# Kernel tuning notes

Measured on AMD Instinct MI355X. Metric: run time of the kernel, lower is better.

Reference implementation:

```python
import jax, jax.numpy as jnp
import numpy as np

H, D, L, G = 4, 32, 2, 512   # heads, head_dim, conv layers, num graphs
HC = H * D                    # hidden_channels = 128


def _mlp3(x, ws, bs):
    # PyG-style MLP, 3 layers, relu between (no act after last), dropout=0
    for i in range(3):
        x = x @ ws[i] + bs[i]
        if i < 2:
            x = jax.nn.relu(x)
    return x


def _attend(q_dst, k_src, v_src, edge, a_rel_et, m_rel_et, p_rel_et, n_dst):
    """One HGTConv edge-type: relation transform, per-dst segment softmax, scatter.
    q_dst: [Nd,H,D], k_src/v_src: [Ns,H,D], edge: [2,E] (src,dst)."""
    src, dst = edge[0], edge[1]
    k_t = jnp.einsum('nhd,hde->nhe', k_src, a_rel_et)   # relation-specific key
    v_t = jnp.einsum('nhd,hde->nhe', v_src, m_rel_et)   # relation-specific value
    alpha = (q_dst[dst] * k_t[src]).sum(-1) * p_rel_et / jnp.sqrt(jnp.float32(D))  # [E,H]
    amax = jax.ops.segment_max(alpha, dst, num_segments=n_dst)
    amax = jnp.where(jnp.isfinite(amax), amax, 0.0)      # nodes with no in-edges
    ex = jnp.exp(alpha - amax[dst])
    den = jax.ops.segment_sum(ex, dst, num_segments=n_dst)
    w = ex / den[dst]                                    # segment softmax weights
    out = jax.ops.segment_sum(v_t[src] * w[..., None], dst, num_segments=n_dst)
    return out.reshape(n_dst, HC)


def _forward(x_var, x_con, mlp_in_w, mlp_in_b,
             mlp_out_w0, mlp_out_b0, mlp_out_w1, mlp_out_b1, mlp_out_w2, mlp_out_b2,
             k_w, k_b, q_w, q_b, v_w, v_b, a_w, a_b, skip,
             a_rel, m_rel, p_rel, edge_vc, edge_cv, batch_var):
    Nv, Nc = x_var.shape[0], x_con.shape[0]
    # per-node-type input MLPs (nt 0 = variable, nt 1 = constraint)
    xs = [_mlp3(x_var, mlp_in_w[0], mlp_in_b[0]),
          _mlp3(x_con, mlp_in_w[1], mlp_in_b[1])]
    ns = [Nv, Nc]
    for l in range(L):  # HGTConv layers
        k = [(xs[t] @ k_w[l, t] + k_b[l, t]).reshape(ns[t], H, D) for t in (0, 1)]
        q = [(xs[t] @ q_w[l, t] + q_b[l, t]).reshape(ns[t], H, D) for t in (0, 1)]
        v = [(xs[t] @ v_w[l, t] + v_b[l, t]).reshape(ns[t], H, D) for t in (0, 1)]
        # edge type 0: variable -> constraint ; edge type 1: constraint -> variable
        agg_con = _attend(q[1], k[0], v[0], edge_vc, a_rel[l, 0], m_rel[l, 0], p_rel[l, 0], Nc)
        agg_var = _attend(q[0], k[1], v[1], edge_cv, a_rel[l, 1], m_rel[l, 1], p_rel[l, 1], Nv)
        # group='mean' over incoming edge types (one per dst type here), then a_lin + gated skip
        new_xs = []
        for t, agg in ((0, agg_var), (1, agg_con)):
            out = jax.nn.gelu(agg, approximate=False) @ a_w[l, t] + a_b[l, t]
            g = jax.nn.sigmoid(skip[l, t])
            new_xs.append(g * out + (1.0 - g) * xs[t])
        xs = new_xs
    # output head on 'variable' nodes: MLP -> softmax(dim=1) -> global mean pool
    logits = _mlp3(xs[0], [mlp_out_w0, mlp_out_w1, mlp_out_w2], [mlp_out_b0, mlp_out_b1, mlp_out_b2])
    probs = jax.nn.softmax(logits, axis=1)
    summ = jax.ops.segment_sum(probs, batch_var, num_segments=G)
    cnt = jax.ops.segment_sum(jnp.ones((xs[0].shape[0],), probs.dtype), batch_var, num_segments=G)
    return summ / jnp.maximum(cnt, 1.0)[:, None]


def setup_inputs() -> dict:
    key = jax.random.key(0)
    ks = jax.random.split(key, 24)
    Nv = Nc = 50000
    E = 400000
    s = 1.0 / np.sqrt(HC)  # fan-in scale for hidden-width linears
    sd = 1.0 / np.sqrt(D)
    inp = {
        'x_var': jax.random.normal(ks[0], (Nv, HC), jnp.float32),
        'x_con': jax.random.normal(ks[1], (Nc, HC), jnp.float32),
        'mlp_in_w': jax.random.normal(ks[2], (2, 3, HC, HC), jnp.float32) * s,
        'mlp_in_b': jnp.zeros((2, 3, HC), jnp.float32),
        'mlp_out_w0': jax.random.normal(ks[3], (HC, HC), jnp.float32) * s,
        'mlp_out_b0': jnp.zeros((HC,), jnp.float32),
        'mlp_out_w1': jax.random.normal(ks[4], (HC, HC), jnp.float32) * s,
        'mlp_out_b1': jnp.zeros((HC,), jnp.float32),
        'mlp_out_w2': jax.random.normal(ks[5], (HC, 2), jnp.float32) * s,
        'mlp_out_b2': jnp.zeros((2,), jnp.float32),
        'k_w': jax.random.normal(ks[6], (L, 2, HC, HC), jnp.float32) * s,
        'k_b': jnp.zeros((L, 2, HC), jnp.float32),
        'q_w': jax.random.normal(ks[7], (L, 2, HC, HC), jnp.float32) * s,
        'q_b': jnp.zeros((L, 2, HC), jnp.float32),
        'v_w': jax.random.normal(ks[8], (L, 2, HC, HC), jnp.float32) * s,
        'v_b': jnp.zeros((L, 2, HC), jnp.float32),
        'a_w': jax.random.normal(ks[9], (L, 2, HC, HC), jnp.float32) * s,
        'a_b': jnp.zeros((L, 2, HC), jnp.float32),
        'skip': jnp.ones((L, 2), jnp.float32),
        'a_rel': jax.random.normal(ks[10], (L, 2, H, D, D), jnp.float32) * sd,
        'm_rel': jax.random.normal(ks[11], (L, 2, H, D, D), jnp.float32) * sd,
        'p_rel': jnp.ones((L, 2, H), jnp.float32),
        'edge_vc': jnp.stack([jax.random.randint(ks[12], (E,), 0, Nv, jnp.int32),
                              jax.random.randint(ks[13], (E,), 0, Nc, jnp.int32)]),
        'edge_cv': jnp.stack([jax.random.randint(ks[14], (E,), 0, Nc, jnp.int32),
                              jax.random.randint(ks[15], (E,), 0, Nv, jnp.int32)]),
        'batch_var': jnp.sort(jax.random.randint(ks[16], (Nv,), 0, G, jnp.int32)),
    }
    return inp


def reference(x_var, x_con, mlp_in_w, mlp_in_b,
              mlp_out_w0, mlp_out_b0, mlp_out_w1, mlp_out_b1, mlp_out_w2, mlp_out_b2,
              k_w, k_b, q_w, q_b, v_w, v_b, a_w, a_b, skip,
              a_rel, m_rel, p_rel, edge_vc, edge_cv, batch_var):
    return _forward(x_var, x_con, mlp_in_w, mlp_in_b,
                    mlp_out_w0, mlp_out_b0, mlp_out_w1, mlp_out_b1, mlp_out_w2, mlp_out_b2,
                    k_w, k_b, q_w, q_b, v_w, v_b, a_w, a_b, skip,
                    a_rel, m_rel, p_rel, edge_vc, edge_cv, batch_var)
```

## Files before the change

kernel.cpp:

```cpp
#include <hip/hip_runtime.h>
#include <cstddef>
#include <cstdint>

typedef __attribute__((ext_vector_type(8))) short short8;
typedef __attribute__((ext_vector_type(4))) float float4v;
typedef __attribute__((ext_vector_type(2))) float float2v;
typedef __attribute__((ext_vector_type(2))) __bf16 bf162;

__device__ __forceinline__ float bf2f_lo(unsigned int u) {
    union { unsigned int i; float f; } v; v.i = u << 16; return v.f;
}
__device__ __forceinline__ float bf2f_hi(unsigned int u) {
    union { unsigned int i; float f; } v; v.i = u & 0xFFFF0000u; return v.f;
}
__device__ __forceinline__ unsigned short f2bf(float f) {
    union { float f; unsigned int i; } v; v.f = f;
    unsigned int x = v.i;
    unsigned int r = (x + 0x7FFFu + ((x >> 16) & 1u)) >> 16;
    return (unsigned short)r;
}
__device__ __forceinline__ float geluf(float x) {
    return 0.5f * x * (1.0f + erff(x * 0.70710678118654752f));
}
__device__ __forceinline__ float dot2bf(unsigned int a, unsigned int b, float c) {
#if defined(__has_builtin) && __has_builtin(__builtin_amdgcn_fdot2_f32_bf16)
    union U { unsigned int u; bf162 v; };
    U ua, ub; ua.u = a; ub.u = b;
    return __builtin_amdgcn_fdot2_f32_bf16(ua.v, ub.v, c, false);
#else
    return c + bf2f_lo(a) * bf2f_lo(b) + bf2f_hi(a) * bf2f_hi(b);
#endif
}
__device__ __forceinline__ unsigned int gate_pack(unsigned int nu, unsigned int ou,
                                                  float2v g2, float2v og2) {
    float2v n = {bf2f_lo(nu), bf2f_hi(nu)};
    float2v o = {bf2f_lo(ou), bf2f_hi(ou)};
    float2v r = n * g2 + o * og2;
    return (unsigned int)f2bf(r.x) | ((unsigned int)f2bf(r.y) << 16);
}

__global__ void k_zero(int* __restrict__ p, int n) {
    int i = blockIdx.x * 256 + threadIdx.x;
    if (i < n) p[i] = 0;
}

__global__ void k_swz(const float* __restrict__ mlp_in_w, const float* __restrict__ q_w,
                      const float* __restrict__ a_w, const float* __restrict__ mow0,
                      const float* __restrict__ mow1, const float* __restrict__ mow2,
                      const float* __restrict__ kw, const float* __restrict__ kb,
                      const float* __restrict__ vw, const float* __restrict__ vb,
                      const float* __restrict__ arel, const float* __restrict__ mrel,
                      const float* __restrict__ prel,
                      unsigned short* __restrict__ Wswz, float* __restrict__ Bkv) {
    int idx = blockIdx.y;
    int f = blockIdx.x * 256 + threadIdx.x;
    if (idx == 25) {
        if (f >= 1024) return;
        int lt = f >> 8, c = f & 255;
        int sec = c >> 7, cc = c & 127, h = cc >> 5, e = cc & 31;
        const float* B = sec ? vb : kb;
        const float* R = sec ? mrel : arel;
        float scale = sec ? 1.f : prel[lt * 4 + h] * 0.17677669529663687f;
        const float* rp = R + (size_t)(lt * 4 + h) * 1024 + e;
        const float* bp = B + lt * 128 + h * 32;
        float s = 0.f;
        #pragma unroll 8
        for (int d = 0; d < 32; ++d) s += bp[d] * rp[(size_t)d * 32];
        Bkv[lt * 256 + c] = s * scale;
        return;
    }
    if (f >= 16384) return;
    int j = f & 7, l = (f >> 3) & 63, t = (f >> 9) & 7, sb = f >> 12;
    int k = sb * 32 + (l >> 4) * 8 + j;
    int n = t * 16 + (l & 15);
    float val;
    if (idx < 6)        val = mlp_in_w[(size_t)idx * 16384 + (size_t)k * 128 + n];
    else if (idx < 10)  val = q_w[(size_t)(idx - 6) * 16384 + (size_t)k * 128 + n];
    else if (idx < 14)  val = a_w[(size_t)(idx - 10) * 16384 + (size_t)k * 128 + n];
    else if (idx == 14) val = mow0[(size_t)k * 128 + n];
    else if (idx == 15) val = mow1[(size_t)k * 128 + n];
    else if (idx < 24) {
        int u = idx - 16, lt = u >> 1, sec = u & 1;
        int h = n >> 5, e = n & 31;
        const float* W = sec ? vw : kw;
        const float* R = sec ? mrel : arel;
        float scale = sec ? 1.f : prel[lt * 4 + h] * 0.17677669529663687f;
        const float* rp = R + (size_t)(lt * 4 + h) * 1024 + e;
        const float* wp = W + (size_t)lt * 16384 + (size_t)k * 128 + h * 32;
        float s = 0.f;
        #pragma unroll 8
        for (int d = 0; d < 32; ++d) s += wp[d] * rp[(size_t)d * 32];
        val = s * scale;
    } else val = (n < 2) ? mow2[(size_t)k * 2 + n] : 0.f;
    Wswz[(size_t)idx * 16384 + f] = f2bf(val);
}

__device__ __forceinline__ void stageB(const unsigned short* __restrict__ Wu,
                                       unsigned short* __restrict__ Bst, int tid) {
    #pragma unroll
    for (int k = 0; k < 8; ++k)
        ((uint4*)Bst)[tid + k * 256] = ((const uint4*)Wu)[tid + k * 256];
}

__device__ __forceinline__ void unit_ldst(const short8 av[4], const unsigned short* __restrict__ Bst,
                                          int lane, float4v acc[8]) {
    #pragma unroll
    for (int t = 0; t < 8; ++t) acc[t] = (float4v){0.f, 0.f, 0.f, 0.f};
    #pragma unroll
    for (int s = 0; s < 4; ++s)
        #pragma unroll
        for (int t = 0; t < 8; ++t) {
            short8 bv = *(const short8*)&Bst[(s * 8 + t) * 512 + lane * 8];
            acc[t] = __builtin_amdgcn_mfma_f32_16x16x32_bf16(av[s], bv, acc[t], 0, 0, 0);
        }
}

__global__ __launch_bounds__(256) void k_mlp3qkv(
    const float* __restrict__ Xa, const float* __restrict__ Xb,
    const unsigned short* __restrict__ Wswz, const float* __restrict__ mlp_in_b,
    const float* __restrict__ q_b, const float* __restrict__ Bkv,
    unsigned short* __restrict__ curS, unsigned short* __restrict__ Qs,
    unsigned short* __restrict__ KVs, int NT, int Nv, int Bv) {
    __shared__ unsigned short Bst[16384];
    __shared__ unsigned short tr[4][16][136];
    const int tid = threadIdx.x;
    const int lane = tid & 63, wave = tid >> 6;
    const int quad = lane >> 4, mrow = lane & 15;
    int bx = blockIdx.x;
    int base, end, type;
    if (bx < Bv) { base = bx * 64; end = Nv; type = 0; }
    else         { base = Nv + (bx - Bv) * 64; end = NT; type = 1; }
    const int mbase = base + wave * 16;
    int r0 = mbase + mrow; if (r0 >= end) r0 = end - 1;
    const bool rok = (mbase + mrow) < end;
    const float* ap = (type == 0 ? Xa + (size_t)r0 * 128
                                 : Xb + (size_t)(r0 - Nv) * 128) + quad * 8;
    short8 av[4];
    #pragma unroll
    for (int s = 0; s < 4; ++s) {
        float4 f0 = *(const float4*)(ap + s * 32);
        float4 f1 = *(const float4*)(ap + s * 32 + 4);
        short8 a;
        a[0] = (short)f2bf(f0.x); a[1] = (short)f2bf(f0.y);
        a[2] = (short)f2bf(f0.z); a[3] = (short)f2bf(f0.w);
        a[4] = (short)f2bf(f1.x); a[5] = (short)f2bf(f1.y);
        a[6] = (short)f2bf(f1.z); a[7] = (short)f2bf(f1.w);
        av[s] = a;
    }
    const float* bs = mlp_in_b + type * 384;
    #pragma unroll
    for (int layer = 0; layer < 3; ++layer) {
        __syncthreads();
        stageB(Wswz + (size_t)(type * 3 + layer) * 16384, Bst, tid);
        __syncthreads();
        float4v acc[8];
        unit_ldst(av, Bst, lane, acc);
        const float* b = bs + layer * 128;
        bool relu = layer < 2;
        #pragma unroll
        for (int t = 0; t < 8; ++t) {
            int col = t * 16 + mrow;
            float bb = b[col];
            #pragma unroll
            for (int r = 0; r < 4; ++r) {
                float v = acc[t][r] + bb;
                if (relu) v = fmaxf(v, 0.f);
                tr[wave][quad * 4 + r][col] = f2bf(v);
            }
        }
        #pragma unroll
        for (int s = 0; s < 4; ++s)
            av[s] = *(const short8*)&tr[wave][mrow][s * 32 + quad * 8];
    }
    if (rok) {
        #pragma unroll
        for (int s = 0; s < 4; ++s)
            *(uint4*)(curS + (size_t)r0 * 128 + quad * 8 + s * 32) = *(uint4*)&av[s];
    }
    #pragma unroll
    for (int u = 0; u < 3; ++u) {
        int unit = (u == 0) ? (6 + type) : (16 + type * 2 + (u - 1));
        __syncthreads();
        stageB(Wswz + (size_t)unit * 16384, Bst, tid);
        __syncthreads();
        float4v acc[8];
        unit_ldst(av, Bst, lane, acc);
        const float* bias = (u == 0) ? (q_b + type * 128) : (Bkv + type * 256 + (u - 1) * 128);
        unsigned short* C = (u == 0) ? Qs : KVs;
        const int ldC = (u == 0) ? 128 : 256;
        const int cb = (u == 0) ? 0 : (u - 1) * 128;
        #pragma unroll
        for (int t = 0; t < 8; ++t) {
            int col = t * 16 + mrow;
            float b = bias[col];
            #pragma unroll
            for (int r = 0; r < 4; ++r) {
                int row = mbase + quad * 4 + r;
                if (row < end) C[(size_t)row * ldC + cb + col] = f2bf(acc[t][r] + b);
            }
        }
    }
}

__global__ __launch_bounds__(256) void k_alinqkv(
    const unsigned short* __restrict__ Aagg, const unsigned short* __restrict__ Wswz,
    const float* __restrict__ a_b, const float* __restrict__ skipP,
    const float* __restrict__ q_b, const float* __restrict__ Bkv,
    unsigned short* __restrict__ curS, unsigned short* __restrict__ Qs,
    unsigned short* __restrict__ KVs, int NT, int Nv, int Bv) {
    __shared__ unsigned short Bst[16384];
    __shared__ unsigned short tr[4][16][136];
    const int tid = threadIdx.x;
    const int lane = tid & 63, wave = tid >> 6;
    const int quad = lane >> 4, mrow = lane & 15;
    int bx = blockIdx.x;
    int base, end, type;
    if (bx < Bv) { base = bx * 64; end = Nv; type = 0; }
    else         { base = Nv + (bx - Bv) * 64; end = NT; type = 1; }
    const int mbase = base + wave * 16;
    int r0 = mbase + mrow; if (r0 >= end) r0 = end - 1;
    const bool rok = (mbase + mrow) < end;
    const int ltA = type;
    const int ltQ = 2 + type;
    short8 av[4];
    {
        const unsigned short* ap = Aagg + (size_t)r0 * 128 + quad * 8;
        #pragma unroll
        for (int s = 0; s < 4; ++s) av[s] = *(const short8*)(ap + s * 32);
    }
    {
        __syncthreads();
        stageB(Wswz + (size_t)(10 + ltA) * 16384, Bst, tid);
        __syncthreads();
        float4v acc[8];
        unit_ldst(av, Bst, lane, acc);
        const float* b = a_b + ltA * 128;
        #pragma unroll
        for (int t = 0; t < 8; ++t) {
            int col = t * 16 + mrow;
            float bb = b[col];
            #pragma unroll
            for (int r = 0; r < 4; ++r)
                tr[wave][quad * 4 + r][col] = f2bf(acc[t][r] + bb);
        }
    }
    {
        float gg = 1.f / (1.f + __expf(-skipP[ltA]));
        float2v g2 = {gg, gg}, og2 = {1.f - gg, 1.f - gg};
        #pragma unroll
        for (int s = 0; s < 4; ++s) {
            short8 nv = *(const short8*)&tr[wave][mrow][s * 32 + quad * 8];
            uint4 nu = *(uint4*)&nv;
            uint4 ou = *(const uint4*)(curS + (size_t)r0 * 128 + quad * 8 + s * 32);
            uint4 res;
            res.x = gate_pack(nu.x, ou.x, g2, og2);
            res.y = gate_pack(nu.y, ou.y, g2, og2);
            res.z = gate_pack(nu.z, ou.z, g2, og2);
            res.w = gate_pack(nu.w, ou.w, g2, og2);
            if (rok) *(uint4*)(curS + (size_t)r0 * 128 + quad * 8 + s * 32) = res;
            av[s] = *(short8*)&res;
        }
    }
    #pragma unroll
    for (int u = 0; u < 3; ++u) {
        int unit = (u == 0) ? (6 + ltQ) : (16 + ltQ * 2 + (u - 1));
        __syncthreads();
        stageB(Wswz + (size_t)unit * 16384, Bst, tid);
        __syncthreads();
        float4v acc[8];
        unit_ldst(av, Bst, lane, acc);
        const float* bias = (u == 0) ? (q_b + ltQ * 128) : (Bkv + ltQ * 256 + (u - 1) * 128);
        unsigned short* C = (u == 0) ? Qs : KVs;
        const int ldC = (u == 0) ? 128 : 256;
        const int cb = (u == 0) ? 0 : (u - 1) * 128;
        #pragma unroll
        for (int t = 0; t < 8; ++t) {
            int col = t * 16 + mrow;
            float b = bias[col];
            #pragma unroll
            for (int r = 0; r < 4; ++r) {
                int row = mbase + quad * 4 + r;
                if (row < end) C[(size_t)row * ldC + cb + col] = f2bf(acc[t][r] + b);
            }
        }
    }
}

__global__ __launch_bounds__(256) void k_alinhead(
    const unsigned short* __restrict__ Aagg, const unsigned short* __restrict__ Wswz,
    const float* __restrict__ a_b, const float* __restrict__ skipP,
    const unsigned short* __restrict__ curS,
    const float* __restrict__ mob0, const float* __restrict__ mob1,
    const float* __restrict__ mob2, const int* __restrict__ batch,
    int N, int G, float* __restrict__ gsum, float* __restrict__ gcnt) {
    __shared__ unsigned short Bst[16384];
    __shared__ unsigned short tr[4][16][136];
    __shared__ float sb[64][3];
    const int tid = threadIdx.x;
    const int lane = tid & 63, wave = tid >> 6;
    const int quad = lane >> 4, mrow = lane & 15;
    for (int i = tid; i < 192; i += 256) ((float*)sb)[i] = 0.f;
    const int base = blockIdx.x * 64;
    const int mbase = base + wave * 16;
    int r0 = mbase + mrow; if (r0 >= N) r0 = N - 1;
    const int bmin = batch[base < N ? base : N - 1];
    short8 av[4];
    {
        const unsigned short* ap = Aagg + (size_t)r0 * 128 + quad * 8;
        #pragma unroll
        for (int s = 0; s < 4; ++s) av[s] = *(const short8*)(ap + s * 32);
    }
    {
        __syncthreads();
        stageB(Wswz + (size_t)12 * 16384, Bst, tid);
        __syncthreads();
        float4v acc[8];
        unit_ldst(av, Bst, lane, acc);
        const float* b = a_b + 2 * 128;
        #pragma unroll
        for (int t = 0; t < 8; ++t) {
            int col = t * 16 + mrow;
            float bb = b[col];
            #pragma unroll
            for (int r = 0; r < 4; ++r)
                tr[wave][quad * 4 + r][col] = f2bf(acc[t][r] + bb);
        }
    }
    {
        float gg = 1.f / (1.f + __expf(-skipP[2]));
        float2v g2 = {gg, gg}, og2 = {1.f - gg, 1.f - gg};
        #pragma unroll
        for (int s = 0; s < 4; ++s) {
            short8 nv = *(const short8*)&tr[wave][mrow][s * 32 + quad * 8];
            uint4 nu = *(uint4*)&nv;
            uint4 ou = *(const uint4*)(curS + (size_t)r0 * 128 + quad * 8 + s * 32);
            uint4 res;
            res.x = gate_pack(nu.x, ou.x, g2, og2);
            res.y = gate_pack(nu.y, ou.y, g2, og2);
            res.z = gate_pack(nu.z, ou.z, g2, og2);
            res.w = gate_pack(nu.w, ou.w, g2, og2);
            av[s] = *(short8*)&res;
        }
    }
    #pragma unroll
    for (int layer = 0; layer < 2; ++layer) {
        __syncthreads();
        stageB(Wswz + (size_t)(14 + layer) * 16384, Bst, tid);
        __syncthreads();
        float4v acc[8];
        unit_ldst(av, Bst, lane, acc);
        const float* b = layer ? mob1 : mob0;
        #pragma unroll
        for (int t = 0; t < 8; ++t) {
            int col = t * 16 + mrow;
            float bb = b[col];
            #pragma unroll
            for (int r = 0; r < 4; ++r)
                tr[wave][quad * 4 + r][col] = f2bf(fmaxf(acc[t][r] + bb, 0.f));
        }
        #pragma unroll
        for (int s = 0; s < 4; ++s)
            av[s] = *(const short8*)&tr[wave][mrow][s * 32 + quad * 8];
    }
    __syncthreads();
    stageB(Wswz + (size_t)24 * 16384, Bst, tid);
    __syncthreads();
    float4v lg = (float4v){0.f, 0.f, 0.f, 0.f};
    #pragma unroll
    for (int s = 0; s < 4; ++s) {
        short8 bv = *(const short8*)&Bst[(s * 8) * 512 + lane * 8];
        lg = __builtin_amdgcn_mfma_f32_16x16x32_bf16(av[s], bv, lg, 0, 0, 0);
    }
    float4v lgo;
    #pragma unroll
    for (int r = 0; r < 4; ++r) lgo[r] = __shfl_xor(lg[r], 1);
    if (mrow == 0) {
        #pragma unroll
        for (int r = 0; r < 4; ++r) {
            int row = mbase + quad * 4 + r;
            if (row < N) {
                float l0 = lg[r] + mob2[0];
                float l1 = lgo[r] + mob2[1];
                float mm = fmaxf(l0, l1);
                float e0 = __expf(l0 - mm), e1 = __expf(l1 - mm);
                float inv = 1.f / (e0 + e1);
                int b = batch[row];
                int rel = b - bmin;
                if (rel >= 0 && rel < 64) {
                    atomicAdd(&sb[rel][0], e0 * inv);
                    atomicAdd(&sb[rel][1], e1 * inv);
                    atomicAdd(&sb[rel][2], 1.f);
                } else {
                    atomicAdd(&gsum[b * 2 + 0], e0 * inv);
                    atomicAdd(&gsum[b * 2 + 1], e1 * inv);
                    atomicAdd(&gcnt[b], 1.f);
                }
            }
        }
    }
    __syncthreads();
    for (int i = tid; i < 64; i += 256) {
        float c = sb[i][2];
        if (c != 0.f && bmin + i < G) {
            atomicAdd(&gsum[(bmin + i) * 2 + 0], sb[i][0]);
            atomicAdd(&gsum[(bmin + i) * 2 + 1], sb[i][1]);
            atomicAdd(&gcnt[bmin + i], c);
        }
    }
}

__global__ void k_hist2(const int* __restrict__ evc, const int* __restrict__ ecv, int E,
                        int* __restrict__ deg, int Nv) {
    int e = blockIdx.x * 256 + threadIdx.x;
    if (e >= E) return;
    if (blockIdx.y == 0) atomicAdd(&deg[Nv + evc[E + e]], 1);
    else                 atomicAdd(&deg[ecv[E + e]], 1);
}
__global__ void k_scan_block(const int* __restrict__ deg, int n, int* __restrict__ off,
                             int* __restrict__ partials) {
    __shared__ int s[256];
    int i = blockIdx.x * 256 + threadIdx.x;
    s[threadIdx.x] = (i < n) ? deg[i] : 0;
    __syncthreads();
    for (int d = 1; d < 256; d <<= 1) {
        int t = (threadIdx.x >= d) ? s[threadIdx.x - d] : 0;
        __syncthreads();
        s[threadIdx.x] += t;
        __syncthreads();
    }
    if (i < n) off[i + 1] = s[threadIdx.x];
    if (threadIdx.x == 255) partials[blockIdx.x] = s[255];
}
__global__ void k_scan_partials(int* __restrict__ partials, int nb) {
    __shared__ int s[512];
    s[threadIdx.x] = (threadIdx.x < nb) ? partials[threadIdx.x] : 0;
    __syncthreads();
    for (int d = 1; d < 512; d <<= 1) {
        int t = (threadIdx.x >= d) ? s[threadIdx.x - d] : 0;
        __syncthreads();
        s[threadIdx.x] += t;
        __syncthreads();
    }
    if (threadIdx.x < nb) partials[threadIdx.x] = s[threadIdx.x];
}
__global__ void k_scan_add(int* __restrict__ off, int* __restrict__ cur,
                           const int* __restrict__ partials, int n) {
    int i = blockIdx.x * 256 + threadIdx.x;
    if (i == 0) { off[0] = 0; cur[0] = 0; }
    if (i < n) {
        int b = i >> 8;
        int v = off[i + 1] + ((b > 0) ? partials[b - 1] : 0);
        off[i + 1] = v;
        cur[i + 1] = v;
    }
}
__global__ void k_scatter2(const int* __restrict__ evc, const int* __restrict__ ecv, int E,
                           int* __restrict__ cur, int Nv, int* __restrict__ srcAll) {
    int e = blockIdx.x * 256 + threadIdx.x;
    if (e >= E) return;
    if (blockIdx.y == 0) {
        int d = Nv + evc[E + e];
        int pos = atomicAdd(&cur[d], 1);
        srcAll[pos] = evc[e];
    } else {
        int d = ecv[E + e];
        int pos = atomicAdd(&cur[d], 1);
        srcAll[pos] = Nv + ecv[e];
    }
}

__global__ __launch_bounds__(256) void k_agg(
    const unsigned short* __restrict__ Q, const unsigned short* __restrict__ KV,
    const int* __restrict__ off, const int* __restrict__ csrc,
    unsigned short* __restrict__ out, int NT) {
    int dst = blockIdx.x * 4 + (threadIdx.x >> 6);
    int lane = threadIdx.x & 63;
    if (dst >= NT) return;
    const int g = lane >> 4, w = lane & 15;
    int2 se = *(const int2*)(off + dst);
    int s0 = se.x, s1 = se.y;
    uint4 qr = *(const uint4*)(Q + (size_t)dst * 128 + w * 8);
    float2v a0 = {0.f, 0.f}, a1 = {0.f, 0.f}, a2 = {0.f, 0.f}, a3 = {0.f, 0.f};
    float den = 0.f;
    int j = s0 + g;
    uint4 kr = {0, 0, 0, 0}, vr = {0, 0, 0, 0};
    bool have = j < s1;
    if (have) {
        const unsigned short* kv = KV + (size_t)csrc[j] * 256 + w * 8;
        kr = *(const uint4*)kv;
        vr = *(const uint4*)(kv + 128);
    }
    while (have) {
        int jn = j + 4;
        bool haveN = jn < s1;
        uint4 krn = kr, vrn = vr;
        if (haveN) {
            const unsigned short* kv = KV + (size_t)csrc[jn] * 256 + w * 8;
            krn = *(const uint4*)kv;
            vrn = *(const uint4*)(kv + 128);
        }
        float t = dot2bf(kr.x, qr.x, 0.f);
        t = dot2bf(kr.y, qr.y, t);
        t = dot2bf(kr.z, qr.z, t);
        t = dot2bf(kr.w, qr.w, t);
        t += __shfl_xor(t, 1);
        t += __shfl_xor(t, 2);
        t = fminf(fmaxf(t, -30.f), 30.f);
        float p = __expf(t);
        den += p;
        float2v pv = {p, p};
        a0 += pv * (float2v){bf2f_lo(vr.x), bf2f_hi(vr.x)};
        a1 += pv * (float2v){bf2f_lo(vr.y), bf2f_hi(vr.y)};
        a2 += pv * (float2v){bf2f_lo(vr.z), bf2f_hi(vr.z)};
        a3 += pv * (float2v){bf2f_lo(vr.w), bf2f_hi(vr.w)};
        kr = krn; vr = vrn; j = jn; have = haveN;
    }
    den += __shfl_xor(den, 16); den += __shfl_xor(den, 32);
    a0.x += __shfl_xor(a0.x, 16); a0.x += __shfl_xor(a0.x, 32);
    a0.y += __shfl_xor(a0.y, 16); a0.y += __shfl_xor(a0.y, 32);
    a1.x += __shfl_xor(a1.x, 16); a1.x += __shfl_xor(a1.x, 32);
    a1.y += __shfl_xor(a1.y, 16); a1.y += __shfl_xor(a1.y, 32);
    a2.x += __shfl_xor(a2.x, 16); a2.x += __shfl_xor(a2.x, 32);
    a2.y += __shfl_xor(a2.y, 16); a2.y += __shfl_xor(a2.y, 32);
    a3.x += __shfl_xor(a3.x, 16); a3.x += __shfl_xor(a3.x, 32);
    a3.y += __shfl_xor(a3.y, 16); a3.y += __shfl_xor(a3.y, 32);
    float inv = (s1 > s0) ? 1.f / den : 0.f;
    float2v r = a0;
    if (g == 1) r = a1;
    if (g == 2) r = a2;
    if (g == 3) r = a3;
    float r0 = geluf(r.x * inv), r1 = geluf(r.y * inv);
    unsigned int o = (unsigned int)f2bf(r0) | ((unsigned int)f2bf(r1) << 16);
    *(unsigned int*)(out + (size_t)dst * 128 + w * 8 + g * 2) = o;
}

__global__ void k_finalize(const float* __restrict__ gsum, const float* __restrict__ gcnt,
                           float* __restrict__ out, int n) {
    int i = blockIdx.x * 256 + threadIdx.x;
    if (i < n) out[i] = gsum[i] / fmaxf(gcnt[i >> 1], 1.f);
}

extern "C" void kernel_launch(void* const* d_in, const int* in_sizes, int n_in,
                              void* d_out, int out_size, void* d_ws, size_t ws_size,
                              hipStream_t stream) {
    const float* x_var    = (const float*)d_in[0];
    const float* x_con    = (const float*)d_in[1];
    const float* mlp_in_w = (const float*)d_in[2];
    const float* mlp_in_b = (const float*)d_in[3];
    const float* mow0 = (const float*)d_in[4];
    const float* mob0 = (const float*)d_in[5];
    const float* mow1 = (const float*)d_in[6];
    const float* mob1 = (const float*)d_in[7];
    const float* mow2 = (const float*)d_in[8];
    const float* mob2 = (const float*)d_in[9];
    const float* k_w  = (const float*)d_in[10];
    const float* k_b  = (const float*)d_in[11];
    const float* q_w  = (const float*)d_in[12];
    const float* q_b  = (const float*)d_in[13];
    const float* v_w  = (const float*)d_in[14];
    const float* v_b  = (const float*)d_in[15];
    const float* a_w  = (const float*)d_in[16];
    const float* a_b  = (const float*)d_in[17];
    const float* skipP = (const float*)d_in[18];
    const float* a_rel = (const float*)d_in[19];
    const float* m_rel = (const float*)d_in[20];
    const float* p_rel = (const float*)d_in[21];
    const int* edge_vc = (const int*)d_in[22];
    const int* edge_cv = (const int*)d_in[23];
    const int* batch   = (const int*)d_in[24];

    const int Nv = in_sizes[0] / 128;
    const int Nc = in_sizes[1] / 128;
    const int E  = in_sizes[22] / 2;
    const int G  = out_size / 2;
    const int NT = Nv + Nc;

    float* fbase = (float*)d_ws;
    size_t fo = 0;
    auto falloc = [&](size_t n) { float* p = fbase + fo; fo += n; return p; };
    float* Bkv  = falloc(4 * 256);
    float* gsum = falloc((size_t)G * 2);
    float* gcnt = falloc((size_t)G);

    unsigned short* bbase = (unsigned short*)(fbase + fo);
    size_t bo = 0;
    auto balloc = [&](size_t n) { unsigned short* p = bbase + bo; bo += n; return p; };
    unsigned short* Wswz = balloc((size_t)25 * 16384);
    unsigned short* curS = balloc((size_t)NT * 128);
    unsigned short* Qs   = balloc((size_t)NT * 128);
    unsigned short* KVs  = balloc((size_t)NT * 256);

    int* ibase = (int*)(bbase + bo);
    size_t io = 0;
    auto ialloc = [&](size_t n) { int* p = ibase + io; io += n; return p; };
    int* offAll = ialloc((size_t)NT + 1);
    int* curAll = ialloc((size_t)NT + 1);
    int* srcAll = ialloc((size_t)E * 2);
    int* deg    = ialloc((size_t)NT);
    int* partials = ialloc(512);

    size_t need = (char*)(ibase + io) - (char*)d_ws;
    if (need > ws_size) return;

    const int eb  = (E + 255) / 256;
    const int nzb = (NT + 255) / 256;
    const int Bv  = (Nv + 63) / 64;
    const int Bc  = (Nc + 63) / 64;

    k_zero<<<nzb, 256, 0, stream>>>(deg, NT);
    k_hist2<<<dim3(eb, 2), 256, 0, stream>>>(edge_vc, edge_cv, E, deg, Nv);
    k_scan_block<<<nzb, 256, 0, stream>>>(deg, NT, offAll, partials);
    k_scan_partials<<<1, 512, 0, stream>>>(partials, nzb);
    k_scan_add<<<nzb, 256, 0, stream>>>(offAll, curAll, partials, NT);
    k_scatter2<<<dim3(eb, 2), 256, 0, stream>>>(edge_vc, edge_cv, E, curAll, Nv, srcAll);

    k_swz<<<dim3(64, 26), 256, 0, stream>>>(mlp_in_w, q_w, a_w, mow0, mow1, mow2,
                                            k_w, k_b, v_w, v_b, a_rel, m_rel, p_rel,
                                            Wswz, Bkv);
    k_zero<<<(G * 3 + 255) / 256, 256, 0, stream>>>((int*)gsum, G * 3);

    k_mlp3qkv<<<Bv + Bc, 256, 0, stream>>>(x_var, x_con, Wswz, mlp_in_b, q_b, Bkv,
                                           curS, Qs, KVs, NT, Nv, Bv);
    k_agg<<<(NT + 3) / 4, 256, 0, stream>>>(Qs, KVs, offAll, srcAll, Qs, NT);
    k_alinqkv<<<Bv + Bc, 256, 0, stream>>>(Qs, Wswz, a_b, skipP, q_b, Bkv,
                                           curS, Qs, KVs, NT, Nv, Bv);
    k_agg<<<(NT + 3) / 4, 256, 0, stream>>>(Qs, KVs, offAll, srcAll, Qs, NT);
    k_alinhead<<<Bv, 256, 0, stream>>>(Qs, Wswz, a_b, skipP, curS,
                                       mob0, mob1, mob2, batch, Nv, G, gsum, gcnt);
    k_finalize<<<(G * 2 + 255) / 256, 256, 0, stream>>>(gsum, gcnt, (float*)d_out, G * 2);
}
```

Before: 508.5 us.

## Prefetch next weight tile into registers and vectorize output stores

In the fused MLP/QKV, update and output kernels, the next weight unit is loaded from global memory into registers while the current unit's MFMA work runs, so weight staging into shared memory overlaps compute. Per-element strided output stores are replaced by a pass through the shared transpose buffer followed by 16-byte vector stores. In the attention aggregation kernel, only one lane per group applies GELU and writes a full uint4, where previously four lanes each wrote 4 bytes. The prefetch adds 8 uint4 registers per thread, which can lower occupancy.

```diff
diff --git a/kernel.cpp b/kernel.cpp
--- a/kernel.cpp
+++ b/kernel.cpp
@@ -18,6 +18,9 @@
     unsigned int x = v.i;
     unsigned int r = (x + 0x7FFFu + ((x >> 16) & 1u)) >> 16;
     return (unsigned short)r;
+}
+__device__ __forceinline__ unsigned int pk2(float lo, float hi) {
+    return (unsigned int)f2bf(lo) | ((unsigned int)f2bf(hi) << 16);
 }
 __device__ __forceinline__ float geluf(float x) {
     return 0.5f * x * (1.0f + erff(x * 0.70710678118654752f));
@@ -36,7 +39,7 @@
     float2v n = {bf2f_lo(nu), bf2f_hi(nu)};
     float2v o = {bf2f_lo(ou), bf2f_hi(ou)};
     float2v r = n * g2 + o * og2;
-    return (unsigned int)f2bf(r.x) | ((unsigned int)f2bf(r.y) << 16);
+    return pk2(r.x, r.y);
 }
 
 __global__ void k_zero(int* __restrict__ p, int n) {
@@ -95,13 +98,6 @@
     Wswz[(size_t)idx * 16384 + f] = f2bf(val);
 }
 
-__device__ __forceinline__ void stageB(const unsigned short* __restrict__ Wu,
-                                       unsigned short* __restrict__ Bst, int tid) {
-    #pragma unroll
-    for (int k = 0; k < 8; ++k)
-        ((uint4*)Bst)[tid + k * 256] = ((const uint4*)Wu)[tid + k * 256];
-}
-
 __device__ __forceinline__ void unit_ldst(const short8 av[4], const unsigned short* __restrict__ Bst,
                                           int lane, float4v acc[8]) {
     #pragma unroll
@@ -133,30 +129,20 @@
     const int mbase = base + wave * 16;
     int r0 = mbase + mrow; if (r0 >= end) r0 = end - 1;
     const bool rok = (mbase + mrow) < end;
-    const float* ap = (type == 0 ? Xa + (size_t)r0 * 128
-                                 : Xb + (size_t)(r0 - Nv) * 128) + quad * 8;
-    short8 av[4];
-    #pragma unroll
-    for (int s = 0; s < 4; ++s) {
-        float4 f0 = *(const float4*)(ap + s * 32);
-        float4 f1 = *(const float4*)(ap + s * 32 + 4);
-        short8 a;
-        a[0] = (short)f2bf(f0.x); a[1] = (short)f2bf(f0.y);
-        a[2] = (short)f2bf(f0.z); a[3] = (short)f2bf(f0.w);
-        a[4] = (short)f2bf(f1.x); a[5] = (short)f2bf(f1.y);
-        a[6] = (short)f2bf(f1.z); a[7] = (short)f2bf(f1.w);
-        av[s] = a;
-    }
-    const float* bs = mlp_in_b + type * 384;
-    #pragma unroll
-    for (int layer = 0; layer < 3; ++layer) {
-        __syncthreads();
-        stageB(Wswz + (size_t)(type * 3 + layer) * 16384, Bst, tid);
-        __syncthreads();
-        float4v acc[8];
-        unit_ldst(av, Bst, lane, acc);
-        const float* b = bs + layer * 128;
-        bool relu = layer < 2;
+
+    const int un[6] = { type * 3, type * 3 + 1, type * 3 + 2,
+                        6 + type, 16 + type * 2, 17 + type * 2 };
+    uint4 pf[8];
+    auto preload = [&](int u) {
+        const uint4* src = (const uint4*)(Wswz + (size_t)u * 16384);
+        #pragma unroll
+        for (int k = 0; k < 8; ++k) pf[k] = src[tid + k * 256];
+    };
+    auto commit = [&]() {
+        #pragma unroll
+        for (int k = 0; k < 8; ++k) ((uint4*)Bst)[tid + k * 256] = pf[k];
+    };
+    auto trwrite = [&](float4v* acc, const float* b, bool relu) {
         #pragma unroll
         for (int t = 0; t < 8; ++t) {
             int col = t * 16 + mrow;
@@ -168,36 +154,58 @@
                 tr[wave][quad * 4 + r][col] = f2bf(v);
             }
         }
-        #pragma unroll
-        for (int s = 0; s < 4; ++s)
-            av[s] = *(const short8*)&tr[wave][mrow][s * 32 + quad * 8];
-    }
-    if (rok) {
-        #pragma unroll
-        for (int s = 0; s < 4; ++s)
-            *(uint4*)(curS + (size_t)r0 * 128 + quad * 8 + s * 32) = *(uint4*)&av[s];
-    }
+    };
+    auto vecstore = [&](unsigned short* C, int ldC, int cb) {
+        if (rok) {
+            #pragma unroll
+            for (int s = 0; s < 4; ++s) {
+                uint4 v = *(const uint4*)&tr[wave][mrow][s * 32 + quad * 8];
+                *(uint4*)(C + (size_t)r0 * ldC + cb + quad * 8 + s * 32) = v;
+            }
+        }
+    };
+
+    short8 av[4];
+    {
+        const float* ap = (type == 0 ? Xa + (size_t)r0 * 128
+                                     : Xb + (size_t)(r0 - Nv) * 128) + quad * 8;
+        #pragma unroll
+        for (int s = 0; s < 4; ++s) {
+            float4 f0 = *(const float4*)(ap + s * 32);
+            float4 f1 = *(const float4*)(ap + s * 32 + 4);
+            short8 a;
+            a[0] = (short)f2bf(f0.x); a[1] = (short)f2bf(f0.y);
+            a[2] = (short)f2bf(f0.z); a[3] = (short)f2bf(f0.w);
+            a[4] = (short)f2bf(f1.x); a[5] = (short)f2bf(f1.y);
+            a[6] = (short)f2bf(f1.z); a[7] = (short)f2bf(f1.w);
+            av[s] = a;
+        }
+    }
+    const float* bs = mlp_in_b + type * 384;
+    preload(un[0]);
     #pragma unroll
-    for (int u = 0; u < 3; ++u) {
-        int unit = (u == 0) ? (6 + type) : (16 + type * 2 + (u - 1));
-        __syncthreads();
-        stageB(Wswz + (size_t)unit * 16384, Bst, tid);
+    for (int ui = 0; ui < 6; ++ui) {
+        __syncthreads();
+        commit();
+        if (ui < 5) preload(un[ui + 1]);
         __syncthreads();
         float4v acc[8];
         unit_ldst(av, Bst, lane, acc);
-        const float* bias = (u == 0) ? (q_b + type * 128) : (Bkv + type * 256 + (u - 1) * 128);
-        unsigned short* C = (u == 0) ? Qs : KVs;
-        const int ldC = (u == 0) ? 128 : 256;
-        const int cb = (u == 0) ? 0 : (u - 1) * 128;
-        #pragma unroll
-        for (int t = 0; t < 8; ++t) {
-            int col = t * 16 + mrow;
-            float b = bias[col];
-            #pragma unroll
-            for (int r = 0; r < 4; ++r) {
-                int row = mbase + quad * 4 + r;
-                if (row < end) C[(size_t)row * ldC + cb + col] = f2bf(acc[t][r] + b);
-            }
+        if (ui < 3) {
+            trwrite(acc, bs + ui * 128, ui < 2);
+            #pragma unroll
+            for (int s = 0; s < 4; ++s)
+                av[s] = *(const short8*)&tr[wave][mrow][s * 32 + quad * 8];
+            if (ui == 2) vecstore(curS, 128, 0);
+        } else if (ui == 3) {
+            trwrite(acc, q_b + type * 128, false);
+            vecstore(Qs, 128, 0);
+        } else if (ui == 4) {
+            trwrite(acc, Bkv + type * 256, false);
+            vecstore(KVs, 256, 0);
+        } else {
+            trwrite(acc, Bkv + type * 256 + 128, false);
+            vecstore(KVs, 256, 128);
         }
     }
 }
@@ -220,68 +228,80 @@
     const int mbase = base + wave * 16;
     int r0 = mbase + mrow; if (r0 >= end) r0 = end - 1;
     const bool rok = (mbase + mrow) < end;
-    const int ltA = type;
-    const int ltQ = 2 + type;
+    const int ltA = type, ltQ = 2 + type;
+    const int un[4] = { 10 + ltA, 6 + ltQ, 16 + ltQ * 2, 17 + ltQ * 2 };
+
+    uint4 pf[8];
+    auto preload = [&](int u) {
+        const uint4* src = (const uint4*)(Wswz + (size_t)u * 16384);
+        #pragma unroll
+        for (int k = 0; k < 8; ++k) pf[k] = src[tid + k * 256];
+    };
+    auto commit = [&]() {
+        #pragma unroll
+        for (int k = 0; k < 8; ++k) ((uint4*)Bst)[tid + k * 256] = pf[k];
+    };
+    auto trwrite = [&](float4v* acc, const float* b) {
+        #pragma unroll
+        for (int t = 0; t < 8; ++t) {
+            int col = t * 16 + mrow;
+            float bb = b[col];
+            #pragma unroll
+            for (int r = 0; r < 4; ++r)
+                tr[wave][quad * 4 + r][col] = f2bf(acc[t][r] + bb);
+        }
+    };
+    auto vecstore = [&](unsigned short* C, int ldC, int cb) {
+        if (rok) {
+            #pragma unroll
+            for (int s = 0; s < 4; ++s) {
+                uint4 v = *(const uint4*)&tr[wave][mrow][s * 32 + quad * 8];
+                *(uint4*)(C + (size_t)r0 * ldC + cb + quad * 8 + s * 32) = v;
+            }
+        }
+    };
+
     short8 av[4];
     {
         const unsigned short* ap = Aagg + (size_t)r0 * 128 + quad * 8;
         #pragma unroll
         for (int s = 0; s < 4; ++s) av[s] = *(const short8*)(ap + s * 32);
     }
-    {
-        __syncthreads();
-        stageB(Wswz + (size_t)(10 + ltA) * 16384, Bst, tid);
+    preload(un[0]);
+    #pragma unroll
+    for (int ui = 0; ui < 4; ++ui) {
+        __syncthreads();
+        commit();
+        if (ui < 3) preload(un[ui + 1]);
         __syncthreads();
         float4v acc[8];
         unit_ldst(av, Bst, lane, acc);
-        const float* b = a_b + ltA * 128;
-        #pragma unroll
-        for (int t = 0; t < 8; ++t) {
-            int col = t * 16 + mrow;
-            float bb = b[col];
-            #pragma unroll
-            for (int r = 0; r < 4; ++r)
-                tr[wave][quad * 4 + r][col] = f2bf(acc[t][r] + bb);
-        }
-    }
-    {
-        float gg = 1.f / (1.f + __expf(-skipP[ltA]));
-        float2v g2 = {gg, gg}, og2 = {1.f - gg, 1.f - gg};
-        #pragma unroll
-        for (int s = 0; s < 4; ++s) {
-            short8 nv = *(const short8*)&tr[wave][mrow][s * 32 + quad * 8];
-            uint4 nu = *(uint4*)&nv;
-            uint4 ou = *(const uint4*)(curS + (size_t)r0 * 128 + quad * 8 + s * 32);
-            uint4 res;
-            res.x = gate_pack(nu.x, ou.x, g2, og2);
-            res.y = gate_pack(nu.y, ou.y, g2, og2);
-            res.z = gate_pack(nu.z, ou.z, g2, og2);
-            res.w = gate_pack(nu.w, ou.w, g2, og2);
-            if (rok) *(uint4*)(curS + (size_t)r0 * 128 + quad * 8 + s * 32) = res;
-            av[s] = *(short8*)&res;
-        }
-    }
-    #pragma unroll
-    for (int u = 0; u < 3; ++u) {
-        int unit = (u == 0) ? (6 + ltQ) : (16 + ltQ * 2 + (u - 1));
-        __syncthreads();
-        stageB(Wswz + (size_t)unit * 16384, Bst, tid);
-        __syncthreads();
-        float4v acc[8];
-        unit_ldst(av, Bst, lane, acc);
-        const float* bias = (u == 0) ? (q_b + ltQ * 128) : (Bkv + ltQ * 256 + (u - 1) * 128);
-        unsigned short* C = (u == 0) ? Qs : KVs;
-        const int ldC = (u == 0) ? 128 : 256;
-        const int cb = (u == 0) ? 0 : (u - 1) * 128;
-        #pragma unroll
-        for (int t = 0; t < 8; ++t) {
-            int col = t * 16 + mrow;
-            float b = bias[col];
-            #pragma unroll
-            for (int r = 0; r < 4; ++r) {
-                int row = mbase + quad * 4 + r;
-                if (row < end) C[(size_t)row * ldC + cb + col] = f2bf(acc[t][r] + b);
-            }
+        if (ui == 0) {
+            trwrite(acc, a_b + ltA * 128);
+            float gg = 1.f / (1.f + __expf(-skipP[ltA]));
+            float2v g2 = {gg, gg}, og2 = {1.f - gg, 1.f - gg};
+            #pragma unroll
+            for (int s = 0; s < 4; ++s) {
+                short8 nv = *(const short8*)&tr[wave][mrow][s * 32 + quad * 8];
+                uint4 nu = *(uint4*)&nv;
+                uint4 ou = *(const uint4*)(curS + (size_t)r0 * 128 + quad * 8 + s * 32);
+                uint4 res;
+                res.x = gate_pack(nu.x, ou.x, g2, og2);
+                res.y = gate_pack(nu.y, ou.y, g2, og2);
+                res.z = gate_pack(nu.z, ou.z, g2, og2);
+                res.w = gate_pack(nu.w, ou.w, g2, og2);
+                if (rok) *(uint4*)(curS + (size_t)r0 * 128 + quad * 8 + s * 32) = res;
+                av[s] = *(short8*)&res;
+            }
+        } else if (ui == 1) {
+            trwrite(acc, q_b + ltQ * 128);
+            vecstore(Qs, 128, 0);
+        } else if (ui == 2) {
+            trwrite(acc, Bkv + ltQ * 256);
+            vecstore(KVs, 256, 0);
+        } else {
+            trwrite(acc, Bkv + ltQ * 256 + 128);
+            vecstore(KVs, 256, 128);
         }
     }
 }
@@ -304,96 +324,99 @@
     const int mbase = base + wave * 16;
     int r0 = mbase + mrow; if (r0 >= N) r0 = N - 1;
     const int bmin = batch[base < N ? base : N - 1];
+    const int un[4] = { 12, 14, 15, 24 };
+
+    uint4 pf[8];
+    auto preload = [&](int u) {
+        const uint4* src = (const uint4*)(Wswz + (size_t)u * 16384);
+        #pragma unroll
+        for (int k = 0; k < 8; ++k) pf[k] = src[tid + k * 256];
+    };
+    auto commit = [&]() {
+        #pragma unroll
+        for (int k = 0; k < 8; ++k) ((uint4*)Bst)[tid + k * 256] = pf[k];
+    };
+
     short8 av[4];
     {
         const unsigned short* ap = Aagg + (size_t)r0 * 128 + quad * 8;
         #pragma unroll
         for (int s = 0; s < 4; ++s) av[s] = *(const short8*)(ap + s * 32);
     }
-    {
-        __syncthreads();
-        stageB(Wswz + (size_t)12 * 16384, Bst, tid);
-        __syncthreads();
-        float4v acc[8];
-        unit_ldst(av, Bst, lane, acc);
-        const float* b = a_b + 2 * 128;
-        #pragma unroll
-        for (int t = 0; t < 8; ++t) {
-            int col = t * 16 + mrow;
-            float bb = b[col];
-            #pragma unroll
-            for (int r = 0; r < 4; ++r)
-                tr[wave][quad * 4 + r][col] = f2bf(acc[t][r] + bb);
-        }
-    }
-    {
-        float gg = 1.f / (1.f + __expf(-skipP[2]));
-        float2v g2 = {gg, gg}, og2 = {1.f - gg, 1.f - gg};
-        #pragma unroll
-        for (int s = 0; s < 4; ++s) {
-            short8 nv = *(const short8*)&tr[wave][mrow][s * 32 + quad * 8];
-            uint4 nu = *(uint4*)&nv;
-            uint4 ou = *(const uint4*)(curS + (size_t)r0 * 128 + quad * 8 + s * 32);
-            uint4 res;
-            res.x = gate_pack(nu.x, ou.x, g2, og2);
-            res.y = gate_pack(nu.y, ou.y, g2, og2);
-            res.z = gate_pack(nu.z, ou.z, g2, og2);
-            res.w = gate_pack(nu.w, ou.w, g2, og2);
-            av[s] = *(short8*)&res;
-        }
-    }
+    preload(un[0]);
     #pragma unroll
-    for (int layer = 0; layer < 2; ++layer) {
-        __syncthreads();
-        stageB(Wswz + (size_t)(14 + layer) * 16384, Bst, tid);
-        __syncthreads();
-        float4v acc[8];
-        unit_ldst(av, Bst, lane, acc);
-        const float* b = layer ? mob1 : mob0;
-        #pragma unroll
-        for (int t = 0; t < 8; ++t) {
-            int col = t * 16 + mrow;
-            float bb = b[col];
-            #pragma unroll
-            for (int r = 0; r < 4; ++r)
-                tr[wave][quad * 4 + r][col] = f2bf(fmaxf(acc[t][r] + bb, 0.f));
-        }
-        #pragma unroll
-        for (int s = 0; s < 4; ++s)
-            av[s] = *(const short8*)&tr[wave][mrow][s * 32 + quad * 8];
-    }
-    __syncthreads();
-    stageB(Wswz + (size_t)24 * 16384, Bst, tid);
-    __syncthreads();
-    float4v lg = (float4v){0.f, 0.f, 0.f, 0.f};
-    #pragma unroll
-    for (int s = 0; s < 4; ++s) {
-        short8 bv = *(const short8*)&Bst[(s * 8) * 512 + lane * 8];
-        lg = __builtin_amdgcn_mfma_f32_16x16x32_bf16(av[s], bv, lg, 0, 0, 0);
-    }
-    float4v lgo;
-    #pragma unroll
-    for (int r = 0; r < 4; ++r) lgo[r] = __shfl_xor(lg[r], 1);
-    if (mrow == 0) {
-        #pragma unroll
-        for (int r = 0; r < 4; ++r) {
-            int row = mbase + quad * 4 + r;
-            if (row < N) {
-                float l0 = lg[r] + mob2[0];
-                float l1 = lgo[r] + mob2[1];
-                float mm = fmaxf(l0, l1);
-                float e0 = __expf(l0 - mm), e1 = __expf(l1 - mm);
-                float inv = 1.f / (e0 + e1);
-                int b = batch[row];
-                int rel = b - bmin;
-                if (rel >= 0 && rel < 64) {
-                    atomicAdd(&sb[rel][0], e0 * inv);
-                    atomicAdd(&sb[rel][1], e1 * inv);
-                    atomicAdd(&sb[rel][2], 1.f);
-                } else {
-                    atomicAdd(&gsum[b * 2 + 0], e0 * inv);
-                    atomicAdd(&gsum[b * 2 + 1], e1 * inv);
-                    atomicAdd(&gcnt[b], 1.f);
+    for (int ui = 0; ui < 4; ++ui) {
+        __syncthreads();
+        commit();
+        if (ui < 3) preload(un[ui + 1]);
+        __syncthreads();
+        if (ui < 3) {
+            float4v acc[8];
+            unit_ldst(av, Bst, lane, acc);
+            const float* b = (ui == 0) ? (a_b + 2 * 128) : (ui == 1 ? mob0 : mob1);
+            #pragma unroll
+            for (int t = 0; t < 8; ++t) {
+                int col = t * 16 + mrow;
+                float bb = b[col];
+                #pragma unroll
+                for (int r = 0; r < 4; ++r) {
+                    float v = acc[t][r] + bb;
+                    if (ui > 0) v = fmaxf(v, 0.f);
+                    tr[wave][quad * 4 + r][col] = f2bf(v);
+                }
+            }
+            if (ui == 0) {
+                float gg = 1.f / (1.f + __expf(-skipP[2]));
+                float2v g2 = {gg, gg}, og2 = {1.f - gg, 1.f - gg};
+                #pragma unroll
+                for (int s = 0; s < 4; ++s) {
+                    short8 nv = *(const short8*)&tr[wave][mrow][s * 32 + quad * 8];
+                    uint4 nu = *(uint4*)&nv;
+                    uint4 ou = *(const uint4*)(curS + (size_t)r0 * 128 + quad * 8 + s * 32);
+                    uint4 res;
+                    res.x = gate_pack(nu.x, ou.x, g2, og2);
+                    res.y = gate_pack(nu.y, ou.y, g2, og2);
+                    res.z = gate_pack(nu.z, ou.z, g2, og2);
+                    res.w = gate_pack(nu.w, ou.w, g2, og2);
+                    av[s] = *(short8*)&res;
+                }
+            } else {
+                #pragma unroll
+                for (int s = 0; s < 4; ++s)
+                    av[s] = *(const short8*)&tr[wave][mrow][s * 32 + quad * 8];
+            }
+        } else {
+            float4v lg = (float4v){0.f, 0.f, 0.f, 0.f};
+            #pragma unroll
+            for (int s = 0; s < 4; ++s) {
+                short8 bv = *(const short8*)&Bst[(s * 8) * 512 + lane * 8];
+                lg = __builtin_amdgcn_mfma_f32_16x16x32_bf16(av[s], bv, lg, 0, 0, 0);
+            }
+            float4v lgo;
+            #pragma unroll
+            for (int r = 0; r < 4; ++r) lgo[r] = __shfl_xor(lg[r], 1);
+            if (mrow == 0) {
+                #pragma unroll
+                for (int r = 0; r < 4; ++r) {
+                    int row = mbase + quad * 4 + r;
+                    if (row < N) {
+                        float l0 = lg[r] + mob2[0];
+                        float l1 = lgo[r] + mob2[1];
+                        float mm = fmaxf(l0, l1);
+                        float e0 = __expf(l0 - mm), e1 = __expf(l1 - mm);
+                        float inv = 1.f / (e0 + e1);
+                        int b = batch[row];
+                        int rel = b - bmin;
+                        if (rel >= 0 && rel < 64) {
+                            atomicAdd(&sb[rel][0], e0 * inv);
+                            atomicAdd(&sb[rel][1], e1 * inv);
+                            atomicAdd(&sb[rel][2], 1.f);
+                        } else {
+                            atomicAdd(&gsum[b * 2 + 0], e0 * inv);
+                            atomicAdd(&gsum[b * 2 + 1], e1 * inv);
+                            atomicAdd(&gcnt[b], 1.f);
+                        }
+                    }
                 }
             }
         }
@@ -524,14 +547,15 @@
     a2.y += __shfl_xor(a2.y, 16); a2.y += __shfl_xor(a2.y, 32);
     a3.x += __shfl_xor(a3.x, 16); a3.x += __shfl_xor(a3.x, 32);
     a3.y += __shfl_xor(a3.y, 16); a3.y += __shfl_xor(a3.y, 32);
-    float inv = (s1 > s0) ? 1.f / den : 0.f;
-    float2v r = a0;
-    if (g == 1) r = a1;
-    if (g == 2) r = a2;
-    if (g == 3) r = a3;
-    float r0 = geluf(r.x * inv), r1 = geluf(r.y * inv);
-    unsigned int o = (unsigned int)f2bf(r0) | ((unsigned int)f2bf(r1) << 16);
-    *(unsigned int*)(out + (size_t)dst * 128 + w * 8 + g * 2) = o;
+    if (g == 0) {
+        float inv = (s1 > s0) ? 1.f / den : 0.f;
+        uint4 o;
+        o.x = pk2(geluf(a0.x * inv), geluf(a0.y * inv));
+        o.y = pk2(geluf(a1.x * inv), geluf(a1.y * inv));
+        o.z = pk2(geluf(a2.x * inv), geluf(a2.y * inv));
+        o.w = pk2(geluf(a3.x * inv), geluf(a3.y * inv));
+        *(uint4*)(out + (size_t)dst * 128 + w * 8) = o;
+    }
 }
 
 __global__ void k_finalize(const float* __restrict__ gsum, const float* __restrict__ gcnt,
```

Result: slower. 608.6 us (+19.7%).
